# Kernel tuning notes

Hardware: AMD Instinct MI355X
Metric: run time of the kernel (lower is better)

## Reference

```python
import jax, jax.numpy as jnp
from jax import lax
import numpy as np

ALPHA = 0.82
MAXITER = 10
N1_NODES = 2048
N2_NODES = 2048
K_ATTR = 64
EDGE_P = 0.004  # sparse-ish adjacency density


def setup_inputs() -> dict:
    key = jax.random.key(0)
    k1, k2, k3, k4 = jax.random.split(key, 4)
    A1 = (jax.random.uniform(k1, (N1_NODES, N1_NODES)) < EDGE_P).astype(jnp.float32)
    A1 = jnp.maximum(A1, A1.T)  # undirected 0/1 adjacency
    A2 = (jax.random.uniform(k2, (N2_NODES, N2_NODES)) < EDGE_P).astype(jnp.float32)
    A2 = jnp.maximum(A2, A2.T)
    N1 = jax.random.uniform(k3, (N1_NODES, K_ATTR), dtype=jnp.float32)
    N2 = jax.random.uniform(k4, (N2_NODES, K_ATTR), dtype=jnp.float32)
    # default prior (_get_H with path=None), normalized so sum ~= 1
    H = jnp.full((N2_NODES, N1_NODES), 1.0 / (N1_NODES * N2_NODES), dtype=jnp.float32)
    return {"A1": A1, "A2": A2, "N1": N1, "N2": N2, "H": H}


def _row_l2_normalize(N):
    nrm = jnp.sqrt(jnp.sum(N * N, axis=1, keepdims=True))
    return jnp.where(nrm > 0, N / jnp.where(nrm > 0, nrm, 1.0), 0.0)


def _final_forward(A1, A2, N1, N2, H, alpha=ALPHA, maxiter=MAXITER):
    # No edge attrs: L=1, E1=A1, E2=A2. T = 1/A^2 where A^2>0 (elementwise),
    # E <- E*T, so B = (E*A) = A*T*A.
    def masked_recip_sq(A):
        A2e = A * A
        return jnp.where(A2e > 0, 1.0 / jnp.where(A2e > 0, A2e, 1.0), 0.0)

    B1 = (A1 * masked_recip_sq(A1)) * A1  # (n1, n1)
    B2 = (A2 * masked_recip_sq(A2)) * A2  # (n2, n2)

    N1n = _row_l2_normalize(N1)  # (n1, K)
    N2n = _row_l2_normalize(N2)  # (n2, K)

    # Kronecker vectors laid out as (n1, n2) matrices (C-order == kron order):
    # N[i*n2+j] = sum_k N1[i,k]*N2[j,k]  -> N1n @ N2n.T
    Nm = N1n @ N2n.T  # (n1, n2)
    dm = (B1 @ N1n) @ (B2 @ N2n).T  # (n1, n2)
    D = Nm * dm
    DD = jnp.where(D > 0, lax.rsqrt(jnp.where(D > 0, D, 1.0)), 0.0)  # inf -> 0
    q = DD * Nm  # (n1, n2)

    # h = H.flatten('F') with H (n2,n1): as an (n1,n2) matrix this is H.T
    h = H.T  # (n1, n2)

    def step(s, _):
        # M = (q*s) reshaped (n2,n1) F-order == (q*s).T in our layout.
        # S = B2 @ M @ B1 (n2,n1); S.flatten('F') as (n1,n2) == B1.T @ (q*s) @ B2.T
        S_t = B1.T @ (q * s) @ B2.T  # (n1, n2)
        s_new = (1.0 - alpha) * h + alpha * q * S_t
        return s_new, None

    s, _ = lax.scan(step, h, None, length=maxiter)
    # original: s.reshape((n1, n2)) C-order -> exactly our layout
    return s  # (n1, n2) alignment matrix


def reference(A1, A2, N1, N2, H):
    return _final_forward(A1, A2, N1, N2, H)
```

## Files before the change

### kernel.cpp

```cpp
#include <hip/hip_runtime.h>

#define NMAT 2048
#define KATTR 64
#define CAP 128
#define NITER 10
#define NSTRIPE 128

typedef unsigned short ushort4v __attribute__((ext_vector_type(4)));

__device__ __forceinline__ unsigned short f2bf(float f) {
  unsigned u = __float_as_uint(f);
  return (unsigned short)((u + 0x7fff + ((u >> 16) & 1)) >> 16);
}
__device__ __forceinline__ float bf2f(unsigned short b) {
  return __uint_as_float((unsigned)b << 16);
}
__device__ __forceinline__ float bflo(unsigned v) {
  return __uint_as_float(v << 16);
}
__device__ __forceinline__ float bfhi(unsigned v) {
  return __uint_as_float(v & 0xffff0000u);
}
__device__ __forceinline__ int swz(int c) { return 4 * c + (((c >> 3) & 7) << 2); }
__device__ __forceinline__ size_t bidx(int i, int j) {
  return ((size_t)(j >> 4) * NMAT + i) * 16 + (j & 15);
}

__global__ __launch_bounds__(256) void k_build(
    const float* __restrict__ A, unsigned short* __restrict__ idx,
    unsigned short* __restrict__ idxT, int* __restrict__ cnt) {
  __shared__ int lcnt;
  int r = blockIdx.x;
  if (threadIdx.x == 0) lcnt = 0;
  __syncthreads();
  const float* row = A + (size_t)r * NMAT;
  for (int c = threadIdx.x; c < NMAT; c += 256) {
    if (row[c] != 0.0f) {
      int p = atomicAdd(&lcnt, 1);
      if (p < CAP) {
        idx[r * CAP + p] = (unsigned short)c;
        if (idxT) idxT[(size_t)p * NMAT + r] = (unsigned short)c;
      }
    }
  }
  __syncthreads();
  if (threadIdx.x == 0) cnt[r] = lcnt < CAP ? lcnt : CAP;
}

__global__ __launch_bounds__(256) void k_norm(const float* __restrict__ Nin,
                                              float* __restrict__ Nout) {
  int row = blockIdx.x * 4 + (threadIdx.x >> 6);
  int lane = threadIdx.x & 63;
  float v = Nin[(size_t)row * KATTR + lane];
  float ss = v * v;
#pragma unroll
  for (int o = 32; o > 0; o >>= 1) ss += __shfl_xor(ss, o);
  float nrm = sqrtf(ss);
  Nout[(size_t)row * KATTR + lane] = (nrm > 0.f) ? v / nrm : 0.f;
}

__global__ void k_gatherN(const unsigned short* __restrict__ idx,
                          const int* __restrict__ cnt,
                          const float* __restrict__ Nn,
                          float* __restrict__ C) {
  int i = blockIdx.x;
  int lane = threadIdx.x;
  int nn = cnt[i];
  const unsigned short* ip = idx + i * CAP;
  float acc = 0.f;
  for (int t = 0; t < nn; ++t) {
    int k = ip[t];
    acc += Nn[(size_t)k * KATTR + lane];
  }
  C[(size_t)i * KATTR + lane] = acc;
}

__global__ __launch_bounds__(256) void k_transpose(const float* __restrict__ H,
                                                   float* __restrict__ Ht) {
  __shared__ float tile[64][65];
  int j0 = blockIdx.x * 64;
  int i0 = blockIdx.y * 64;
  int c = threadIdx.x & 63;
  int r0 = threadIdx.x >> 6;
  for (int r = r0; r < 64; r += 4)
    tile[r][c] = H[(size_t)(j0 + r) * NMAT + i0 + c];
  __syncthreads();
  for (int r = r0; r < 64; r += 4)
    Ht[(size_t)(i0 + r) * NMAT + j0 + c] = tile[c][r];
}

__global__ __launch_bounds__(256) void k_q(
    const float* __restrict__ N1n, const float* __restrict__ C1,
    const float* __restrict__ N2n, const float* __restrict__ C2,
    const float* __restrict__ Ht, float* __restrict__ q,
    float* __restrict__ Q2, unsigned short* __restrict__ Mblk,
    unsigned short* __restrict__ M0base) {
  __shared__ float sA[64][68];
  __shared__ float sB[64][68];
  int i0 = blockIdx.y * 64, j0 = blockIdx.x * 64;
  int c = threadIdx.x & 63, r0 = threadIdx.x >> 6;
  int tx = threadIdx.x & 15, ty = threadIdx.x >> 4;
  const float alpha = 0.82f;

  float nmv[4][4] = {};
  float dmv[4][4] = {};

  for (int r = r0; r < 64; r += 4) {
    sA[c][r] = N1n[(size_t)(i0 + r) * KATTR + c];
    sB[c][r] = N2n[(size_t)(j0 + r) * KATTR + c];
  }
  __syncthreads();
#pragma unroll 4
  for (int k = 0; k < 64; ++k) {
    float4 a = *(const float4*)&sA[k][ty * 4];
    float4 b = *(const float4*)&sB[k][tx * 4];
    float av[4] = {a.x, a.y, a.z, a.w};
    float bv[4] = {b.x, b.y, b.z, b.w};
#pragma unroll
    for (int ii = 0; ii < 4; ++ii)
#pragma unroll
      for (int jj = 0; jj < 4; ++jj)
        nmv[ii][jj] = fmaf(av[ii], bv[jj], nmv[ii][jj]);
  }
  __syncthreads();
  for (int r = r0; r < 64; r += 4) {
    sA[c][r] = C1[(size_t)(i0 + r) * KATTR + c];
    sB[c][r] = C2[(size_t)(j0 + r) * KATTR + c];
  }
  __syncthreads();
#pragma unroll 4
  for (int k = 0; k < 64; ++k) {
    float4 a = *(const float4*)&sA[k][ty * 4];
    float4 b = *(const float4*)&sB[k][tx * 4];
    float av[4] = {a.x, a.y, a.z, a.w};
    float bv[4] = {b.x, b.y, b.z, b.w};
#pragma unroll
    for (int ii = 0; ii < 4; ++ii)
#pragma unroll
      for (int jj = 0; jj < 4; ++jj)
        dmv[ii][jj] = fmaf(av[ii], bv[jj], dmv[ii][jj]);
  }

#pragma unroll
  for (int ii = 0; ii < 4; ++ii) {
    int i = i0 + ty * 4 + ii;
    int jb = j0 + tx * 4;
    size_t base = (size_t)i * NMAT + jb;
    float4 hv = *(const float4*)&Ht[base];
    float hvv[4] = {hv.x, hv.y, hv.z, hv.w};
    float qv[4], q2v[4];
    ushort4v mv, m0v;
#pragma unroll
    for (int jj = 0; jj < 4; ++jj) {
      float nmx = nmv[ii][jj];
      float D = nmx * dmv[ii][jj];
      float qq = (D > 0.f) ? nmx * rsqrtf(D) : 0.f;
      qv[jj] = qq;
      q2v[jj] = alpha * qq * qq;
      float m0 = qq * hvv[jj];
      mv[jj] = f2bf(m0);
      m0v[jj] = f2bf((1.0f - alpha) * m0);
    }
    *(float4*)&q[base] = make_float4(qv[0], qv[1], qv[2], qv[3]);
    *(float4*)&Q2[base] = make_float4(q2v[0], q2v[1], q2v[2], q2v[3]);
    *(ushort4v*)&Mblk[bidx(i, jb)] = mv;
    *(ushort4v*)&M0base[base] = m0v;
  }
}

__global__ __launch_bounds__(1024, 8) void k1s(
    const unsigned short* __restrict__ idx1, const int* __restrict__ cnt1,
    const unsigned short* __restrict__ Mblk, float* __restrict__ T1) {
  __shared__ __align__(16) unsigned lds[NMAT * 8];
  int stripe = blockIdx.x & (NSTRIPE - 1);
  int chunk = blockIdx.x >> 7;
  int tid = threadIdx.x;
  const unsigned* src = (const unsigned*)(Mblk + (size_t)stripe * NMAT * 16);
#pragma unroll
  for (int p = 0; p < 4; ++p) {
    int e = p * 4096 + tid * 4;
    *(uint4*)&lds[e] = *(const uint4*)(src + e);
  }
  __syncthreads();

  int i = chunk * 512 + (tid >> 1);
  int h = tid & 1;
  int nn = cnt1[i];
  const unsigned short* ip = idx1 + i * CAP;
  float a0 = 0, a1 = 0, a2 = 0, a3 = 0, a4 = 0, a5 = 0, a6 = 0, a7 = 0;
  int hh = h * 4;
  int t = 0;
  for (; t + 2 <= nn; t += 2) {
    unsigned pr = *(const unsigned*)(ip + t);
    uint4 w = *(const uint4*)&lds[(int)(pr & 0xffff) * 8 + hh];
    uint4 x = *(const uint4*)&lds[(int)(pr >> 16) * 8 + hh];
    a0 += bflo(w.x) + bflo(x.x); a1 += bfhi(w.x) + bfhi(x.x);
    a2 += bflo(w.y) + bflo(x.y); a3 += bfhi(w.y) + bfhi(x.y);
    a4 += bflo(w.z) + bflo(x.z); a5 += bfhi(w.z) + bfhi(x.z);
    a6 += bflo(w.w) + bflo(x.w); a7 += bfhi(w.w) + bfhi(x.w);
  }
  if (t < nn) {
    uint4 w = *(const uint4*)&lds[(int)ip[t] * 8 + hh];
    a0 += bflo(w.x); a1 += bfhi(w.x);
    a2 += bflo(w.y); a3 += bfhi(w.y);
    a4 += bflo(w.z); a5 += bfhi(w.z);
    a6 += bflo(w.w); a7 += bfhi(w.w);
  }
  float* dst = T1 + (size_t)i * NMAT + stripe * 16 + h * 8;
  *(float4*)dst = make_float4(a0, a1, a2, a3);
  *(float4*)(dst + 4) = make_float4(a4, a5, a6, a7);
}

__global__ __launch_bounds__(1024, 8) void k2s(
    const unsigned short* __restrict__ idx2T, const int* __restrict__ cnt2,
    const float* __restrict__ T1, const float* __restrict__ Q2,
    const unsigned short* __restrict__ M0base,
    unsigned short* __restrict__ Moutb, float* __restrict__ MoutF,
    int out32) {
  __shared__ float lds[4 * NMAT + 32];
  int i0 = blockIdx.x * 4;
  int tid = threadIdx.x;
  int c0 = tid * 2;
  float2 v[4];
#pragma unroll
  for (int r = 0; r < 4; ++r)
    v[r] = *(const float2*)(T1 + (size_t)(i0 + r) * NMAT + c0);
  *(float4*)&lds[swz(c0)] = make_float4(v[0].x, v[1].x, v[2].x, v[3].x);
  *(float4*)&lds[swz(c0 + 1)] = make_float4(v[0].y, v[1].y, v[2].y, v[3].y);
  __syncthreads();

#pragma unroll
  for (int jj = 0; jj < 2; ++jj) {
    int j = jj * 1024 + tid;
    int nn = cnt2[j];
    const unsigned short* ip = idx2T + j;
    float s0 = 0.f, s1 = 0.f, s2 = 0.f, s3 = 0.f;
    float u0 = 0.f, u1 = 0.f, u2 = 0.f, u3 = 0.f;
    int t = 0;
    for (; t + 4 <= nn; t += 4) {
      int ka = ip[(size_t)t * NMAT];
      int kb = ip[(size_t)(t + 1) * NMAT];
      int kc = ip[(size_t)(t + 2) * NMAT];
      int kd = ip[(size_t)(t + 3) * NMAT];
      float4 va = *(const float4*)&lds[swz(ka)];
      float4 vb = *(const float4*)&lds[swz(kb)];
      float4 vc = *(const float4*)&lds[swz(kc)];
      float4 vd = *(const float4*)&lds[swz(kd)];
      s0 += va.x + vc.x; s1 += va.y + vc.y;
      s2 += va.z + vc.z; s3 += va.w + vc.w;
      u0 += vb.x + vd.x; u1 += vb.y + vd.y;
      u2 += vb.z + vd.z; u3 += vb.w + vd.w;
    }
    for (; t < nn; ++t) {
      int ka = ip[(size_t)t * NMAT];
      float4 va = *(const float4*)&lds[swz(ka)];
      s0 += va.x; s1 += va.y; s2 += va.z; s3 += va.w;
    }
    float sa[4] = {s0 + u0, s1 + u1, s2 + u2, s3 + u3};
    if (out32) {
#pragma unroll
      for (int r = 0; r < 4; ++r) {
        size_t off = (size_t)(i0 + r) * NMAT + j;
        MoutF[off] = fmaf(Q2[off], sa[r], bf2f(M0base[off]));
      }
    } else {
#pragma unroll
      for (int r = 0; r < 4; ++r) {
        size_t off = (size_t)(i0 + r) * NMAT + j;
        Moutb[bidx(i0 + r, j)] = f2bf(fmaf(Q2[off], sa[r], bf2f(M0base[off])));
      }
    }
  }
}

__global__ __launch_bounds__(1024, 8) void k_iter(
    const unsigned short* __restrict__ idx1, const int* __restrict__ cnt1,
    const unsigned short* __restrict__ idx2T, const int* __restrict__ cnt2,
    const float* __restrict__ MinF, const float* __restrict__ q,
    const float* __restrict__ Ht, float* __restrict__ sout) {
  __shared__ float lds[4 * NMAT + 32];
  int i0 = blockIdx.x * 4;
  int tid = threadIdx.x;
  int c0 = tid * 2;

  float acc[4][2];
#pragma unroll
  for (int r = 0; r < 4; ++r) {
    int nn = cnt1[i0 + r];
    const unsigned short* ip = idx1 + (i0 + r) * CAP;
    float a0 = 0.f, a1 = 0.f;
    float b0 = 0.f, b1 = 0.f;
    int t = 0;
    for (; t + 4 <= nn; t += 4) {
      uint2 pk = *(const uint2*)(ip + t);
      int k0 = pk.x & 0xffff, k1 = pk.x >> 16;
      int k2 = pk.y & 0xffff, k3 = pk.y >> 16;
      float2 v0 = *(const float2*)(MinF + (size_t)k0 * NMAT + c0);
      float2 v1 = *(const float2*)(MinF + (size_t)k1 * NMAT + c0);
      float2 v2 = *(const float2*)(MinF + (size_t)k2 * NMAT + c0);
      float2 v3 = *(const float2*)(MinF + (size_t)k3 * NMAT + c0);
      a0 += v0.x + v1.x; a1 += v0.y + v1.y;
      b0 += v2.x + v3.x; b1 += v2.y + v3.y;
    }
    for (; t < nn; ++t) {
      float2 v0 = *(const float2*)(MinF + (size_t)ip[t] * NMAT + c0);
      a0 += v0.x; a1 += v0.y;
    }
    acc[r][0] = a0 + b0;
    acc[r][1] = a1 + b1;
  }
  *(float4*)&lds[swz(c0)] =
      make_float4(acc[0][0], acc[1][0], acc[2][0], acc[3][0]);
  *(float4*)&lds[swz(c0 + 1)] =
      make_float4(acc[0][1], acc[1][1], acc[2][1], acc[3][1]);
  __syncthreads();

  const float alpha = 0.82f;
  const float oma = 1.0f - alpha;
#pragma unroll
  for (int jj = 0; jj < 2; ++jj) {
    int j = jj * 1024 + tid;
    int nn = cnt2[j];
    const unsigned short* ip = idx2T + j;
    float s0 = 0.f, s1 = 0.f, s2 = 0.f, s3 = 0.f;
    float u0 = 0.f, u1 = 0.f, u2 = 0.f, u3 = 0.f;
    int t = 0;
    for (; t + 4 <= nn; t += 4) {
      int ka = ip[(size_t)t * NMAT];
      int kb = ip[(size_t)(t + 1) * NMAT];
      int kc = ip[(size_t)(t + 2) * NMAT];
      int kd = ip[(size_t)(t + 3) * NMAT];
      float4 va = *(const float4*)&lds[swz(ka)];
      float4 vb = *(const float4*)&lds[swz(kb)];
      float4 vc = *(const float4*)&lds[swz(kc)];
      float4 vd = *(const float4*)&lds[swz(kd)];
      s0 += va.x + vc.x; s1 += va.y + vc.y;
      s2 += va.z + vc.z; s3 += va.w + vc.w;
      u0 += vb.x + vd.x; u1 += vb.y + vd.y;
      u2 += vb.z + vd.z; u3 += vb.w + vd.w;
    }
    for (; t < nn; ++t) {
      int ka = ip[(size_t)t * NMAT];
      float4 va = *(const float4*)&lds[swz(ka)];
      s0 += va.x; s1 += va.y; s2 += va.z; s3 += va.w;
    }
    float sa[4] = {s0 + u0, s1 + u1, s2 + u2, s3 + u3};
#pragma unroll
    for (int r = 0; r < 4; ++r) {
      size_t off = (size_t)(i0 + r) * NMAT + j;
      sout[off] = oma * Ht[off] + alpha * q[off] * sa[r];
    }
  }
}

extern "C" void kernel_launch(void* const* d_in, const int* in_sizes, int n_in,
                              void* d_out, int out_size, void* d_ws,
                              size_t ws_size, hipStream_t stream) {
  const float* A1 = (const float*)d_in[0];
  const float* A2 = (const float*)d_in[1];
  const float* N1 = (const float*)d_in[2];
  const float* N2 = (const float*)d_in[3];
  const float* H = (const float*)d_in[4];
  float* s_out = (float*)d_out;

  char* p = (char*)d_ws;
  auto take = [&](size_t bytes) {
    char* r = p;
    p += (bytes + 255) & ~(size_t)255;
    return r;
  };
  unsigned short* idx1 = (unsigned short*)take((size_t)NMAT * CAP * 2);
  unsigned short* idx2 = (unsigned short*)take((size_t)NMAT * CAP * 2);
  unsigned short* idx2T = (unsigned short*)take((size_t)CAP * NMAT * 2);
  int* cnt1 = (int*)take((size_t)NMAT * 4);
  int* cnt2 = (int*)take((size_t)NMAT * 4);
  float* N1n = (float*)take((size_t)NMAT * KATTR * 4);
  float* N2n = (float*)take((size_t)NMAT * KATTR * 4);
  float* C1 = (float*)take((size_t)NMAT * KATTR * 4);
  float* C2 = (float*)take((size_t)NMAT * KATTR * 4);
  float* Ht = (float*)take((size_t)NMAT * NMAT * 4);
  float* q = (float*)take((size_t)NMAT * NMAT * 4);
  float* Q2 = (float*)take((size_t)NMAT * NMAT * 4);
  unsigned short* Mb0 = (unsigned short*)take((size_t)NMAT * NMAT * 2);
  unsigned short* Mb1 = (unsigned short*)take((size_t)NMAT * NMAT * 2);
  unsigned short* M0b = (unsigned short*)take((size_t)NMAT * NMAT * 2);
  float* Mf = (float*)take((size_t)NMAT * NMAT * 4);
  float* T1 = (float*)take((size_t)NMAT * NMAT * 4);
  if ((size_t)(p - (char*)d_ws) > ws_size) return;

  k_build<<<NMAT, 256, 0, stream>>>(A1, idx1, (unsigned short*)nullptr, cnt1);
  k_build<<<NMAT, 256, 0, stream>>>(A2, idx2, idx2T, cnt2);
  k_norm<<<NMAT / 4, 256, 0, stream>>>(N1, N1n);
  k_norm<<<NMAT / 4, 256, 0, stream>>>(N2, N2n);
  k_gatherN<<<NMAT, 64, 0, stream>>>(idx1, cnt1, N1n, C1);
  k_gatherN<<<NMAT, 64, 0, stream>>>(idx2, cnt2, N2n, C2);
  k_transpose<<<dim3(32, 32), 256, 0, stream>>>(H, Ht);
  k_q<<<dim3(32, 32), 256, 0, stream>>>(N1n, C1, N2n, C2, Ht, q, Q2, Mb0,
                                        M0b);
  for (int it = 0; it < NITER - 1; ++it) {
    const unsigned short* Min = (it & 1) ? Mb1 : Mb0;
    unsigned short* Mout = (it & 1) ? Mb0 : Mb1;
    int out32 = (it == NITER - 2) ? 1 : 0;
    k1s<<<4 * NSTRIPE, 1024, 0, stream>>>(idx1, cnt1, Min, T1);
    k2s<<<NMAT / 4, 1024, 0, stream>>>(idx2T, cnt2, T1, Q2, M0b, Mout, Mf,
                                       out32);
  }
  k_iter<<<NMAT / 4, 1024, 0, stream>>>(idx1, cnt1, idx2T, cnt2, Mf, q, Ht,
                                        s_out);
}
```

Before: 465.0 us.

## Run last two iterations in fp32 and replace atomic row compaction with prefix scan

The final two propagation iterations now run through the fp32 fused k_iter kernel instead of one bf16 k1s/k2s pair plus the final step. This adds a second fp32 buffer and more fp32 traffic but reduces bf16 rounding in late iterations. Separately, k_build replaces the per-element shared atomic with a per-thread count and a block prefix scan, which produces deterministic, column-ordered index lists. The scan adds many barriers to a setup kernel that runs only twice.

New measurement: 477.4 us. +2.7%, slower.

```diff
diff --git a/kernel.cpp b/kernel.cpp
--- a/kernel.cpp
+++ b/kernel.cpp
@@ -29,22 +29,40 @@
 __global__ __launch_bounds__(256) void k_build(
     const float* __restrict__ A, unsigned short* __restrict__ idx,
     unsigned short* __restrict__ idxT, int* __restrict__ cnt) {
-  __shared__ int lcnt;
+  __shared__ int pre[256];
   int r = blockIdx.x;
-  if (threadIdx.x == 0) lcnt = 0;
-  __syncthreads();
+  int tid = threadIdx.x;
   const float* row = A + (size_t)r * NMAT;
-  for (int c = threadIdx.x; c < NMAT; c += 256) {
+  int c0 = tid * 8;
+  int cl = 0;
+#pragma unroll
+  for (int e = 0; e < 8; ++e) cl += (row[c0 + e] != 0.0f) ? 1 : 0;
+  pre[tid] = cl;
+  __syncthreads();
+#pragma unroll
+  for (int off = 1; off < 256; off <<= 1) {
+    int t = (tid >= off) ? pre[tid - off] : 0;
+    __syncthreads();
+    pre[tid] += t;
+    __syncthreads();
+  }
+  int excl = pre[tid] - cl;
+  int p = excl;
+#pragma unroll
+  for (int e = 0; e < 8; ++e) {
+    int c = c0 + e;
     if (row[c] != 0.0f) {
-      int p = atomicAdd(&lcnt, 1);
       if (p < CAP) {
         idx[r * CAP + p] = (unsigned short)c;
         if (idxT) idxT[(size_t)p * NMAT + r] = (unsigned short)c;
       }
-    }
-  }
-  __syncthreads();
-  if (threadIdx.x == 0) cnt[r] = lcnt < CAP ? lcnt : CAP;
+      ++p;
+    }
+  }
+  if (tid == 0) {
+    int total = pre[255];
+    cnt[r] = total < CAP ? total : CAP;
+  }
 }
 
 __global__ __launch_bounds__(256) void k_norm(const float* __restrict__ Nin,
@@ -276,8 +294,10 @@
 __global__ __launch_bounds__(1024, 8) void k_iter(
     const unsigned short* __restrict__ idx1, const int* __restrict__ cnt1,
     const unsigned short* __restrict__ idx2T, const int* __restrict__ cnt2,
-    const float* __restrict__ MinF, const float* __restrict__ q,
-    const float* __restrict__ Ht, float* __restrict__ sout) {
+    const float* __restrict__ MinF, const float* __restrict__ Q2,
+    const unsigned short* __restrict__ M0base, const float* __restrict__ q,
+    const float* __restrict__ Ht, float* __restrict__ MoutF,
+    float* __restrict__ sout, int last) {
   __shared__ float lds[4 * NMAT + 32];
   int i0 = blockIdx.x * 4;
   int tid = threadIdx.x;
@@ -345,10 +365,18 @@
       s0 += va.x; s1 += va.y; s2 += va.z; s3 += va.w;
     }
     float sa[4] = {s0 + u0, s1 + u1, s2 + u2, s3 + u3};
-#pragma unroll
-    for (int r = 0; r < 4; ++r) {
-      size_t off = (size_t)(i0 + r) * NMAT + j;
-      sout[off] = oma * Ht[off] + alpha * q[off] * sa[r];
+    if (last) {
+#pragma unroll
+      for (int r = 0; r < 4; ++r) {
+        size_t off = (size_t)(i0 + r) * NMAT + j;
+        sout[off] = oma * Ht[off] + alpha * q[off] * sa[r];
+      }
+    } else {
+#pragma unroll
+      for (int r = 0; r < 4; ++r) {
+        size_t off = (size_t)(i0 + r) * NMAT + j;
+        MoutF[off] = fmaf(Q2[off], sa[r], bf2f(M0base[off]));
+      }
     }
   }
 }
@@ -384,7 +412,8 @@
   unsigned short* Mb0 = (unsigned short*)take((size_t)NMAT * NMAT * 2);
   unsigned short* Mb1 = (unsigned short*)take((size_t)NMAT * NMAT * 2);
   unsigned short* M0b = (unsigned short*)take((size_t)NMAT * NMAT * 2);
-  float* Mf = (float*)take((size_t)NMAT * NMAT * 4);
+  float* Mf0 = (float*)take((size_t)NMAT * NMAT * 4);
+  float* Mf1 = (float*)take((size_t)NMAT * NMAT * 4);
   float* T1 = (float*)take((size_t)NMAT * NMAT * 4);
   if ((size_t)(p - (char*)d_ws) > ws_size) return;
 
@@ -397,14 +426,16 @@
   k_transpose<<<dim3(32, 32), 256, 0, stream>>>(H, Ht);
   k_q<<<dim3(32, 32), 256, 0, stream>>>(N1n, C1, N2n, C2, Ht, q, Q2, Mb0,
                                         M0b);
-  for (int it = 0; it < NITER - 1; ++it) {
+  for (int it = 0; it < 8; ++it) {
     const unsigned short* Min = (it & 1) ? Mb1 : Mb0;
     unsigned short* Mout = (it & 1) ? Mb0 : Mb1;
-    int out32 = (it == NITER - 2) ? 1 : 0;
+    int out32 = (it == 7) ? 1 : 0;
     k1s<<<4 * NSTRIPE, 1024, 0, stream>>>(idx1, cnt1, Min, T1);
-    k2s<<<NMAT / 4, 1024, 0, stream>>>(idx2T, cnt2, T1, Q2, M0b, Mout, Mf,
+    k2s<<<NMAT / 4, 1024, 0, stream>>>(idx2T, cnt2, T1, Q2, M0b, Mout, Mf0,
                                        out32);
   }
-  k_iter<<<NMAT / 4, 1024, 0, stream>>>(idx1, cnt1, idx2T, cnt2, Mf, q, Ht,
-                                        s_out);
-}
+  k_iter<<<NMAT / 4, 1024, 0, stream>>>(idx1, cnt1, idx2T, cnt2, Mf0, Q2,
+                                        M0b, q, Ht, Mf1, s_out, 0);
+  k_iter<<<NMAT / 4, 1024, 0, stream>>>(idx1, cnt1, idx2T, cnt2, Mf1, Q2,
+                                        M0b, q, Ht, Mf0, s_out, 1);
+}
```
